# Kernel optimization log

Hardware: AMD Instinct MI355X
Metric: run time of the kernel (lower is better)

## Reference

```python
import jax, jax.numpy as jnp
import numpy as np

TEMPERATURE = 0.03


def setup_inputs() -> dict:
    key = jax.random.key(0)
    k1, k2, k3 = jax.random.split(key, 3)
    B, d = 8192, 256
    z_a = jax.random.normal(k1, (B, d), dtype=jnp.float32)
    z_t = jax.random.normal(k2, (B, d), dtype=jnp.float32)
    # module expects L2-normalized projections
    z_a = z_a / jnp.linalg.norm(z_a, axis=-1, keepdims=True)
    z_t = z_t / jnp.linalg.norm(z_t, axis=-1, keepdims=True)
    patient_ids = jax.random.randint(k3, (B,), 0, 2048, dtype=jnp.int64)
    return {"z_a": z_a, "z_t": z_t, "patient_ids": patient_ids}


def _direction_loss(sim, cross_mask):
    # sim: (B, B) row i = anchor i vs all candidates; cross_mask: (B, B) valid negatives
    B = sim.shape[0]
    pos = jnp.diagonal(sim)                              # (B,) positive logits
    logit_mask = cross_mask | jnp.eye(B, dtype=bool)     # negatives + the positive
    lse = jax.nn.logsumexp(sim, axis=1, where=logit_mask)  # (B,)
    row_loss = lse - pos                                 # CE with label = positive
    valid = cross_mask.any(axis=1)                       # rows with >=1 cross-patient neg
    cnt = jnp.sum(valid)
    total = jnp.sum(jnp.where(valid, row_loss, 0.0))
    return jnp.where(cnt > 0, total / jnp.maximum(cnt, 1).astype(sim.dtype), 0.0)


def reference(z_a, z_t, patient_ids):
    sim = jnp.matmul(z_a, z_t.T) / TEMPERATURE           # (B, B)
    cross = patient_ids[:, None] != patient_ids[None, :] # cross-patient negative mask
    loss_a2t = _direction_loss(sim, cross)
    loss_t2a = _direction_loss(sim.T, cross.T)
    return (loss_a2t + loss_t2a) / 2.0
```

## Files before the change

### kernel.cpp

```cpp
#include <hip/hip_runtime.h>
#include <math.h>

#define BSZ    8192
#define DDIM   256
#define SCALE  33.33333333333333f
#define C_OFF  34.0f
#define SC_L2E 48.08983470f
#define C2     49.05163139f

typedef float floatx4 __attribute__((ext_vector_type(4)));
typedef long long fp8x8;

__device__ __forceinline__ fp8x8 cvt8_f8(const float* __restrict__ g)
{
    const float4 lo = *(const float4*)g;
    const float4 hi = *(const float4*)(g + 4);
    int a = __builtin_amdgcn_cvt_pk_fp8_f32(lo.x, lo.y, 0, false);
    a     = __builtin_amdgcn_cvt_pk_fp8_f32(lo.z, lo.w, a, true);
    int b = __builtin_amdgcn_cvt_pk_fp8_f32(hi.x, hi.y, 0, false);
    b     = __builtin_amdgcn_cvt_pk_fp8_f32(hi.z, hi.w, b, true);
    int2 r; r.x = a; r.y = b;
    return *(fp8x8*)&r;
}

__global__ __launch_bounds__(256) void prep_kernel(
    const float* __restrict__ za, const float* __restrict__ zt,
    unsigned char* __restrict__ za_f8, unsigned char* __restrict__ zt_perm,
    float* __restrict__ zbase)
{
    const int bid = blockIdx.x, tid = threadIdx.x;
    if (bid < 1024) {
        const int i = (bid * 256 + tid) * 8;
        *(fp8x8*)(za_f8 + i) = cvt8_f8(za + i);
        if (bid < 16) {
            const int z = bid * 1024 + tid * 4;
            *(float4*)&zbase[z] = (float4){0.f, 0.f, 0.f, 0.f};
            if (bid == 0 && tid == 0) {
                zbase[16384] = 0.f;
                ((int*)zbase)[16385] = 0;
                ((int*)zbase)[16386] = 0;
            }
        }
    } else {
        const int S     = (bid - 1024) * 256 + tid;
        const int chunk = S >> 9, P = S & 511;
        const int col   = P >> 2, sp = P & 3;
        const int sl    = sp ^ ((col >> 2) & 3);
        const int cb    = chunk >> 3, kc = chunk & 7;
        const float* src = zt + (size_t)(cb * 128 + col) * DDIM + kc * 32 + sl * 8;
        *(fp8x8*)(zt_perm + (size_t)S * 8) = cvt8_f8(src);
    }
}

__global__ __launch_bounds__(256, 2) void sim_fused(
    const unsigned char* __restrict__ za_f8, const unsigned char* __restrict__ zt_perm,
    const int* __restrict__ pid,
    float* __restrict__ s_row, float* __restrict__ s_col,
    float* __restrict__ posv)
{
    __shared__ int   pidc[512];
    __shared__ float colsum[512];

    const int bid   = blockIdx.x;
    const int strip = bid & 15, band = bid >> 4;
    const int row0  = band * 128, scol0 = strip * 512;
    const int tid   = threadIdx.x, lane = tid & 63, wid = tid >> 6;
    const int q     = lane >> 4, lc = lane & 15;
    const int rbase = row0 + wid * 32;
    const int qs8   = (q ^ ((lc >> 2) & 3)) * 8;

    pidc[tid]         = pid[scol0 + tid];
    pidc[tid + 256]   = pid[scol0 + tid + 256];
    colsum[tid]       = 0.f;
    colsum[tid + 256] = 0.f;

    fp8x8 af[2][8];
    #pragma unroll
    for (int m = 0; m < 2; m++) {
        const unsigned char* ga = za_f8 + (size_t)(rbase + m * 16 + lc) * DDIM + q * 8;
        #pragma unroll
        for (int kc = 0; kc < 8; kc++)
            af[m][kc] = *(const fp8x8*)(ga + kc * 32);
    }

    int prw[2][4];
    #pragma unroll
    for (int m = 0; m < 2; m++)
        #pragma unroll
        for (int r = 0; r < 4; r++)
            prw[m][r] = pid[rbase + m * 16 + q * 4 + r];

    __syncthreads();

    const unsigned char* bb = zt_perm + (size_t)strip * 131072 + lc * 32 + qs8;

    float rowp[8] = {0.f, 0.f, 0.f, 0.f, 0.f, 0.f, 0.f, 0.f};
    const int diag_t = (row0 - scol0) >> 7;

    for (int t = 0; t < 4; t++) {
        floatx4 acc[2][8];
        #pragma unroll
        for (int m = 0; m < 2; m++)
            #pragma unroll
            for (int n = 0; n < 8; n++)
                acc[m][n] = (floatx4){0.f, 0.f, 0.f, 0.f};

        #pragma unroll
        for (int c2 = 0; c2 < 2; c2++) {
            const unsigned char* bc = bb + (size_t)(t * 2 + c2) * 16384;
            #pragma unroll
            for (int j = 0; j < 4; j++) {
                const int kc = c2 * 4 + j;
                fp8x8 bfr[8];
                #pragma unroll
                for (int n = 0; n < 8; n++)
                    bfr[n] = *(const fp8x8*)(bc + j * 4096 + n * 512);

                #pragma unroll
                for (int m = 0; m < 2; m++)
                    #pragma unroll
                    for (int n = 0; n < 8; n++)
                        acc[m][n] = __builtin_amdgcn_mfma_f32_16x16x32_fp8_fp8(
                            af[m][kc], bfr[n], acc[m][n], 0, 0, 0);
            }
        }

        int pc[8];
        #pragma unroll
        for (int n = 0; n < 8; n++) pc[n] = pidc[t * 128 + n * 16 + lc];

        float colp[8] = {0.f, 0.f, 0.f, 0.f, 0.f, 0.f, 0.f, 0.f};
        #pragma unroll
        for (int m = 0; m < 2; m++) {
            #pragma unroll
            for (int r = 0; r < 4; r++) {
                const int pr = prw[m][r];
                float rsum = 0.f;
                #pragma unroll
                for (int n = 0; n < 8; n++) {
                    float e = __builtin_amdgcn_exp2f(fmaf(acc[m][n][r], SC_L2E, -C2));
                    e = (pr != pc[n]) ? e : 0.f;
                    rsum += e;
                    colp[n] += e;
                }
                rowp[m * 4 + r] += rsum;
            }
        }

        if (t == diag_t) {
            #pragma unroll
            for (int m = 0; m < 2; m++) {
                const int nstar = wid * 2 + m;
                #pragma unroll
                for (int r = 0; r < 4; r++) {
                    float v = 0.f;
                    #pragma unroll
                    for (int n = 0; n < 8; n++)
                        v = (n == nstar) ? acc[m][n][r] : v;
                    float e = __builtin_amdgcn_exp2f(fmaf(v, SC_L2E, -C2));
                    const bool own = (lc == q * 4 + r);
                    e = own ? e : 0.f;
                    rowp[m * 4 + r] += e;
                    #pragma unroll
                    for (int n = 0; n < 8; n++)
                        colp[n] += (n == nstar) ? e : 0.f;
                    if (own) posv[rbase + m * 16 + q * 4 + r] = v * SCALE;
                }
            }
        }

        #pragma unroll
        for (int n = 0; n < 8; n++) {
            colp[n] += __shfl_xor(colp[n], 16, 64);
            colp[n] += __shfl_xor(colp[n], 32, 64);
        }
        if (q == 0) {
            #pragma unroll
            for (int n = 0; n < 8; n++)
                atomicAdd(&colsum[t * 128 + n * 16 + lc], colp[n]);
        }
    }

    #pragma unroll
    for (int i = 0; i < 8; i++) {
        rowp[i] += __shfl_xor(rowp[i], 1, 64);
        rowp[i] += __shfl_xor(rowp[i], 2, 64);
        rowp[i] += __shfl_xor(rowp[i], 4, 64);
        rowp[i] += __shfl_xor(rowp[i], 8, 64);
    }
    float rw = rowp[0];
    #pragma unroll
    for (int idx = 1; idx < 8; idx++)
        rw = (lc == idx) ? rowp[idx] : rw;
    if (lc < 8)
        atomicAdd(&s_row[rbase + (lc >> 2) * 16 + q * 4 + (lc & 3)], rw);

    __syncthreads();
    atomicAdd(&s_col[scol0 + tid], colsum[tid]);
    atomicAdd(&s_col[scol0 + tid + 256], colsum[tid + 256]);
}

__global__ __launch_bounds__(256) void finalize_rows(
    const int* __restrict__ pid,
    const float* __restrict__ s_row, const float* __restrict__ s_col,
    const float* __restrict__ posv,
    float* __restrict__ total, int* __restrict__ flag, int* __restrict__ cnt,
    float* __restrict__ out)
{
    const int i = blockIdx.x * 256 + threadIdx.x;
    const float p = posv[i];
    const float c = (logf(s_row[i]) + C_OFF - p)
                  + (logf(s_col[i]) + C_OFF - p);

    float v = c;
    #pragma unroll
    for (int off = 32; off > 0; off >>= 1) v += __shfl_down(v, off, 64);
    if ((threadIdx.x & 63) == 0) atomicAdd(total, v);

    const unsigned long long m = __ballot(pid[i] != pid[0]);
    if (m != 0ull && (threadIdx.x & 63) == 0) atomicOr(flag, 1);

    __syncthreads();
    __threadfence();
    if (threadIdx.x == 0) {
        const int done = atomicAdd(cnt, 1);
        if (done == (int)gridDim.x - 1) {
            const float t = atomicAdd(total, 0.0f);
            const int   f = atomicOr(flag, 0);
            out[0] = f ? t / (2.0f * (float)BSZ) : 0.0f;
        }
    }
}

extern "C" void kernel_launch(void* const* d_in, const int* in_sizes, int n_in,
                              void* d_out, int out_size, void* d_ws, size_t ws_size,
                              hipStream_t stream)
{
    const float* za  = (const float*)d_in[0];
    const float* zt  = (const float*)d_in[1];
    const int*   pid = (const int*)d_in[2];
    float* out = (float*)d_out;

    unsigned char* za_f8   = (unsigned char*)d_ws;
    unsigned char* zt_perm = za_f8 + (size_t)BSZ * DDIM;
    float*  s_row   = (float*)(zt_perm + (size_t)BSZ * DDIM);
    float*  s_col   = s_row + BSZ;
    float*  total   = s_col + BSZ;
    int*    flag    = (int*)(total + 1);
    int*    cnt     = flag + 1;
    float*  posv    = (float*)(cnt + 1);

    prep_kernel<<<dim3(2048), 256, 0, stream>>>(za, zt, za_f8, zt_perm, s_row);

    sim_fused<<<dim3(1024), 256, 0, stream>>>(za_f8, zt_perm, pid,
                                              s_row, s_col, posv);

    finalize_rows<<<dim3(BSZ / 256), 256, 0, stream>>>(
        pid, s_row, s_col, posv, total, flag, cnt, out);
}
```

Measured before the change: 125.7 us.

## Retile sim kernel to 128x128 blocks with LDS-staged B via direct global-to-LDS loads

Each block now computes a 128x128 tile with a 2x2 wave grid of 64x64 subtiles, instead of a 128x512 strip with each wave covering 32 rows. The B tile is staged in shared memory with global_load_lds, so the waves share it instead of each reading it from global memory. The grid grows from 1024 to 4096 blocks. This raises parallelism and cuts redundant global B reads, but adds more atomics on s_row and s_col, 32KB of LDS per block, and reloading of A fragments per tile.

```diff
diff --git a/kernel.cpp b/kernel.cpp
--- a/kernel.cpp
+++ b/kernel.cpp
@@ -58,131 +58,128 @@
     float* __restrict__ s_row, float* __restrict__ s_col,
     float* __restrict__ posv)
 {
-    __shared__ int   pidc[512];
-    __shared__ float colsum[512];
-
-    const int bid   = blockIdx.x;
-    const int strip = bid & 15, band = bid >> 4;
-    const int row0  = band * 128, scol0 = strip * 512;
-    const int tid   = threadIdx.x, lane = tid & 63, wid = tid >> 6;
-    const int q     = lane >> 4, lc = lane & 15;
-    const int rbase = row0 + wid * 32;
+    __shared__ __align__(16) unsigned char Bs[32768];
+    __shared__ int   pidc[128];
+    __shared__ float colsum[128];
+
+    const int bid  = blockIdx.x;
+    const int cb   = bid & 63, band = bid >> 6;
+    const int row0 = band * 128, col0 = cb * 128;
+    const int tid  = threadIdx.x, lane = tid & 63, wid = tid >> 6;
+    const int wr   = wid >> 1, wc = wid & 1;
+    const int q    = lane >> 4, lc = lane & 15;
+    const int rbase = row0 + wr * 64;
     const int qs8   = (q ^ ((lc >> 2) & 3)) * 8;
 
-    pidc[tid]         = pid[scol0 + tid];
-    pidc[tid + 256]   = pid[scol0 + tid + 256];
-    colsum[tid]       = 0.f;
-    colsum[tid + 256] = 0.f;
-
-    fp8x8 af[2][8];
-    #pragma unroll
-    for (int m = 0; m < 2; m++) {
+    if (tid < 128) { pidc[tid] = pid[col0 + tid]; colsum[tid] = 0.f; }
+
+    {
+        const unsigned char* src = zt_perm + (size_t)cb * 32768 + wid * 8192 + lane * 16;
+        unsigned char* dst = Bs + wid * 8192 + lane * 16;
+        #pragma unroll
+        for (int i = 0; i < 8; i++)
+            __builtin_amdgcn_global_load_lds(
+                (const __attribute__((address_space(1))) void*)(src + i * 1024),
+                (__attribute__((address_space(3))) void*)(dst + i * 1024),
+                16, 0, 0);
+    }
+
+    fp8x8 af[4][8];
+    #pragma unroll
+    for (int m = 0; m < 4; m++) {
         const unsigned char* ga = za_f8 + (size_t)(rbase + m * 16 + lc) * DDIM + q * 8;
         #pragma unroll
         for (int kc = 0; kc < 8; kc++)
             af[m][kc] = *(const fp8x8*)(ga + kc * 32);
     }
 
-    int prw[2][4];
-    #pragma unroll
-    for (int m = 0; m < 2; m++)
+    int prw[4][4];
+    #pragma unroll
+    for (int m = 0; m < 4; m++)
         #pragma unroll
         for (int r = 0; r < 4; r++)
             prw[m][r] = pid[rbase + m * 16 + q * 4 + r];
 
     __syncthreads();
 
-    const unsigned char* bb = zt_perm + (size_t)strip * 131072 + lc * 32 + qs8;
-
-    float rowp[8] = {0.f, 0.f, 0.f, 0.f, 0.f, 0.f, 0.f, 0.f};
-    const int diag_t = (row0 - scol0) >> 7;
-
-    for (int t = 0; t < 4; t++) {
-        floatx4 acc[2][8];
-        #pragma unroll
-        for (int m = 0; m < 2; m++)
+    const unsigned char* bb = Bs + wc * 2048 + lc * 32 + qs8;
+
+    floatx4 acc[4][4];
+    #pragma unroll
+    for (int m = 0; m < 4; m++)
+        #pragma unroll
+        for (int n = 0; n < 4; n++)
+            acc[m][n] = (floatx4){0.f, 0.f, 0.f, 0.f};
+
+    #pragma unroll
+    for (int kc = 0; kc < 8; kc++) {
+        fp8x8 bfr[4];
+        #pragma unroll
+        for (int n = 0; n < 4; n++)
+            bfr[n] = *(const fp8x8*)(bb + kc * 4096 + n * 512);
+        #pragma unroll
+        for (int m = 0; m < 4; m++)
             #pragma unroll
-            for (int n = 0; n < 8; n++)
-                acc[m][n] = (floatx4){0.f, 0.f, 0.f, 0.f};
-
-        #pragma unroll
-        for (int c2 = 0; c2 < 2; c2++) {
-            const unsigned char* bc = bb + (size_t)(t * 2 + c2) * 16384;
+            for (int n = 0; n < 4; n++)
+                acc[m][n] = __builtin_amdgcn_mfma_f32_16x16x32_fp8_fp8(
+                    af[m][kc], bfr[n], acc[m][n], 0, 0, 0);
+    }
+
+    int pc[4];
+    #pragma unroll
+    for (int n = 0; n < 4; n++) pc[n] = pidc[wc * 64 + n * 16 + lc];
+
+    float rowp[16];
+    #pragma unroll
+    for (int i = 0; i < 16; i++) rowp[i] = 0.f;
+    float colp[4] = {0.f, 0.f, 0.f, 0.f};
+
+    #pragma unroll
+    for (int m = 0; m < 4; m++) {
+        #pragma unroll
+        for (int r = 0; r < 4; r++) {
+            const int pr = prw[m][r];
+            float rsum = 0.f;
             #pragma unroll
-            for (int j = 0; j < 4; j++) {
-                const int kc = c2 * 4 + j;
-                fp8x8 bfr[8];
-                #pragma unroll
-                for (int n = 0; n < 8; n++)
-                    bfr[n] = *(const fp8x8*)(bc + j * 4096 + n * 512);
-
-                #pragma unroll
-                for (int m = 0; m < 2; m++)
-                    #pragma unroll
-                    for (int n = 0; n < 8; n++)
-                        acc[m][n] = __builtin_amdgcn_mfma_f32_16x16x32_fp8_fp8(
-                            af[m][kc], bfr[n], acc[m][n], 0, 0, 0);
+            for (int n = 0; n < 4; n++) {
+                float e = __builtin_amdgcn_exp2f(fmaf(acc[m][n][r], SC_L2E, -C2));
+                e = (pr != pc[n]) ? e : 0.f;
+                rsum += e;
+                colp[n] += e;
             }
-        }
-
-        int pc[8];
-        #pragma unroll
-        for (int n = 0; n < 8; n++) pc[n] = pidc[t * 128 + n * 16 + lc];
-
-        float colp[8] = {0.f, 0.f, 0.f, 0.f, 0.f, 0.f, 0.f, 0.f};
-        #pragma unroll
-        for (int m = 0; m < 2; m++) {
+            rowp[m * 4 + r] += rsum;
+        }
+    }
+
+    if (band == cb && wr == wc) {
+        #pragma unroll
+        for (int m = 0; m < 4; m++) {
             #pragma unroll
             for (int r = 0; r < 4; r++) {
-                const int pr = prw[m][r];
-                float rsum = 0.f;
-                #pragma unroll
-                for (int n = 0; n < 8; n++) {
-                    float e = __builtin_amdgcn_exp2f(fmaf(acc[m][n][r], SC_L2E, -C2));
-                    e = (pr != pc[n]) ? e : 0.f;
-                    rsum += e;
-                    colp[n] += e;
-                }
-                rowp[m * 4 + r] += rsum;
+                const float v = acc[m][m][r];
+                float e = __builtin_amdgcn_exp2f(fmaf(v, SC_L2E, -C2));
+                const bool own = (lc == q * 4 + r);
+                e = own ? e : 0.f;
+                rowp[m * 4 + r] += e;
+                colp[m] += e;
+                if (own) posv[rbase + m * 16 + q * 4 + r] = v * SCALE;
             }
         }
-
-        if (t == diag_t) {
-            #pragma unroll
-            for (int m = 0; m < 2; m++) {
-                const int nstar = wid * 2 + m;
-                #pragma unroll
-                for (int r = 0; r < 4; r++) {
-                    float v = 0.f;
-                    #pragma unroll
-                    for (int n = 0; n < 8; n++)
-                        v = (n == nstar) ? acc[m][n][r] : v;
-                    float e = __builtin_amdgcn_exp2f(fmaf(v, SC_L2E, -C2));
-                    const bool own = (lc == q * 4 + r);
-                    e = own ? e : 0.f;
-                    rowp[m * 4 + r] += e;
-                    #pragma unroll
-                    for (int n = 0; n < 8; n++)
-                        colp[n] += (n == nstar) ? e : 0.f;
-                    if (own) posv[rbase + m * 16 + q * 4 + r] = v * SCALE;
-                }
-            }
-        }
-
-        #pragma unroll
-        for (int n = 0; n < 8; n++) {
-            colp[n] += __shfl_xor(colp[n], 16, 64);
-            colp[n] += __shfl_xor(colp[n], 32, 64);
-        }
-        if (q == 0) {
-            #pragma unroll
-            for (int n = 0; n < 8; n++)
-                atomicAdd(&colsum[t * 128 + n * 16 + lc], colp[n]);
-        }
-    }
-
-    #pragma unroll
-    for (int i = 0; i < 8; i++) {
+    }
+
+    #pragma unroll
+    for (int n = 0; n < 4; n++) {
+        colp[n] += __shfl_xor(colp[n], 16, 64);
+        colp[n] += __shfl_xor(colp[n], 32, 64);
+    }
+    if (q == 0) {
+        #pragma unroll
+        for (int n = 0; n < 4; n++)
+            atomicAdd(&colsum[wc * 64 + n * 16 + lc], colp[n]);
+    }
+
+    #pragma unroll
+    for (int i = 0; i < 16; i++) {
         rowp[i] += __shfl_xor(rowp[i], 1, 64);
         rowp[i] += __shfl_xor(rowp[i], 2, 64);
         rowp[i] += __shfl_xor(rowp[i], 4, 64);
@@ -190,14 +187,12 @@
     }
     float rw = rowp[0];
     #pragma unroll
-    for (int idx = 1; idx < 8; idx++)
+    for (int idx = 1; idx < 16; idx++)
         rw = (lc == idx) ? rowp[idx] : rw;
-    if (lc < 8)
-        atomicAdd(&s_row[rbase + (lc >> 2) * 16 + q * 4 + (lc & 3)], rw);
+    atomicAdd(&s_row[rbase + (lc >> 2) * 16 + q * 4 + (lc & 3)], rw);
 
     __syncthreads();
-    atomicAdd(&s_col[scol0 + tid], colsum[tid]);
-    atomicAdd(&s_col[scol0 + tid + 256], colsum[tid + 256]);
+    if (tid < 128) atomicAdd(&s_col[col0 + tid], colsum[tid]);
 }
 
 __global__ __launch_bounds__(256) void finalize_rows(
@@ -252,7 +247,7 @@
 
     prep_kernel<<<dim3(2048), 256, 0, stream>>>(za, zt, za_f8, zt_perm, s_row);
 
-    sim_fused<<<dim3(1024), 256, 0, stream>>>(za_f8, zt_perm, pid,
+    sim_fused<<<dim3(4096), 256, 0, stream>>>(za_f8, zt_perm, pid,
                                               s_row, s_col, posv);
 
     finalize_rows<<<dim3(BSZ / 256), 256, 0, stream>>>(
```

Measured after the change: 144.3 us. 14.9% more time.

## Stream B operand through per-wave LDS double buffer via async global_load_lds

Applied to the files above, without the earlier changes.

Replaces direct global fp8x8 loads of the z_t operand with per-wave asynchronous global-to-LDS copies into a two-slot buffer, prefetching two k-chunks ahead and gating with explicit vmcnt/lgkmcnt waits. The aim is to hide global memory latency behind the MFMA work instead of stalling on each B fragment load. It adds 32 KB of LDS per block, which may limit occupancy at two blocks per CU, and relies on hand-placed waitcnt counts and on the address mapping matching the old permuted layout, so there is a correctness risk.

```diff
diff --git a/kernel.cpp b/kernel.cpp
--- a/kernel.cpp
+++ b/kernel.cpp
@@ -58,6 +58,7 @@
     float* __restrict__ s_row, float* __restrict__ s_col,
     float* __restrict__ posv)
 {
+    __shared__ __align__(16) unsigned char Bs[4][8192];
     __shared__ int   pidc[512];
     __shared__ float colsum[512];
 
@@ -74,6 +75,24 @@
     colsum[tid]       = 0.f;
     colsum[tid + 256] = 0.f;
 
+    const unsigned char* zp = zt_perm + (size_t)strip * 131072 + lane * 16;
+    unsigned char* wbuf = &Bs[wid][0];
+
+#define WSTAGE(so, doff)                                                         \
+    do {                                                                         \
+        const unsigned char* _s = zp + (so);                                     \
+        unsigned char* _d = wbuf + (doff);                                       \
+        _Pragma("unroll")                                                        \
+        for (int _i = 0; _i < 4; _i++)                                           \
+            __builtin_amdgcn_global_load_lds(                                    \
+                (const __attribute__((address_space(1))) void*)(_s + _i * 1024), \
+                (__attribute__((address_space(3))) void*)(_d + _i * 1024),       \
+                16, 0, 0);                                                       \
+    } while (0)
+
+    WSTAGE(0, 0);
+    WSTAGE(16384, 4096);
+
     fp8x8 af[2][8];
     #pragma unroll
     for (int m = 0; m < 2; m++) {
@@ -92,8 +111,6 @@
 
     __syncthreads();
 
-    const unsigned char* bb = zt_perm + (size_t)strip * 131072 + lc * 32 + qs8;
-
     float rowp[8] = {0.f, 0.f, 0.f, 0.f, 0.f, 0.f, 0.f, 0.f};
     const int diag_t = (row0 - scol0) >> 7;
 
@@ -106,23 +123,32 @@
                 acc[m][n] = (floatx4){0.f, 0.f, 0.f, 0.f};
 
         #pragma unroll
-        for (int c2 = 0; c2 < 2; c2++) {
-            const unsigned char* bc = bb + (size_t)(t * 2 + c2) * 16384;
-            #pragma unroll
-            for (int j = 0; j < 4; j++) {
-                const int kc = c2 * 4 + j;
-                fp8x8 bfr[8];
+        for (int kc = 0; kc < 8; kc++) {
+            if (kc == 7 && t == 3)
+                __asm__ volatile("s_waitcnt vmcnt(0)" ::: "memory");
+            else
+                __asm__ volatile("s_waitcnt vmcnt(4)" ::: "memory");
+
+            const unsigned char* B = wbuf + (kc & 1) * 4096;
+            fp8x8 bfr[8];
+            #pragma unroll
+            for (int n = 0; n < 8; n++)
+                bfr[n] = *(const fp8x8*)(B + (n * 16 + lc) * 32 + qs8);
+
+            __asm__ volatile("s_waitcnt lgkmcnt(0)" ::: "memory");
+            {
+                const int c2 = t * 8 + kc + 2;
+                if (c2 < 32)
+                    WSTAGE(((size_t)(c2 & 7)) * 16384 + ((size_t)(c2 >> 3)) * 4096,
+                           (kc & 1) * 4096);
+            }
+
+            #pragma unroll
+            for (int m = 0; m < 2; m++)
                 #pragma unroll
                 for (int n = 0; n < 8; n++)
-                    bfr[n] = *(const fp8x8*)(bc + j * 4096 + n * 512);
-
-                #pragma unroll
-                for (int m = 0; m < 2; m++)
-                    #pragma unroll
-                    for (int n = 0; n < 8; n++)
-                        acc[m][n] = __builtin_amdgcn_mfma_f32_16x16x32_fp8_fp8(
-                            af[m][kc], bfr[n], acc[m][n], 0, 0, 0);
-            }
+                    acc[m][n] = __builtin_amdgcn_mfma_f32_16x16x32_fp8_fp8(
+                        af[m][kc], bfr[n], acc[m][n], 0, 0, 0);
         }
 
         int pc[8];
@@ -198,6 +224,7 @@
     __syncthreads();
     atomicAdd(&s_col[scol0 + tid], colsum[tid]);
     atomicAdd(&s_col[scol0 + tid + 256], colsum[tid + 256]);
+#undef WSTAGE
 }
 
 __global__ __launch_bounds__(256) void finalize_rows(
```

Result: no change. 125.9 us (+0.2%).
